# Performance work log

Hardware: AMD Instinct MI355X
Metric: run time of the kernel (lower is better)

The kernel has to match this reference:

```python
import jax, jax.numpy as jnp
import numpy as np

M_RANGE = 3
K = 2 * M_RANGE + 1          # kernel size = 7
N_CLASS = K * K              # 49 motion classes
IM_CHANNEL = 3


def setup_inputs() -> dict:
    key = jax.random.key(0)
    k1, k2, k3, k4 = jax.random.split(key, 4)
    B, H, W = 16, 256, 256
    im_input = jax.random.normal(k1, (B, 2 * IM_CHANNEL, H, W), dtype=jnp.float32)
    im_output = jax.random.normal(k2, (B, IM_CHANNEL, H, W), dtype=jnp.float32)
    # motion in [-M_RANGE, M_RANGE-1) so that floor(m)+M_RANGE+1 <= K-1 (valid bin)
    gt_motion = jax.random.uniform(k3, (B, 2, H, W), dtype=jnp.float32) * (2 * M_RANGE - 1) - M_RANGE
    # grouped-conv weight (already in post-swapaxes [n_class, 1, K, K] layout)
    m_kernel = jax.random.uniform(k4, (N_CLASS, 1, K, K), dtype=jnp.float32)
    return {"im_input": im_input, "im_output": im_output,
            "gt_motion": gt_motion, "m_kernel": m_kernel}


def _axis_weights(m):
    # m: [B,H,W] -> bilinear binning weights over K bins: [B,H,W,K]
    f = jnp.floor(m)
    frac = m - f
    idx = f.astype(jnp.int32) + M_RANGE
    oh0 = jax.nn.one_hot(idx, K, dtype=m.dtype)
    oh1 = jax.nn.one_hot(idx + 1, K, dtype=m.dtype)
    return (1.0 - frac)[..., None] * oh0 + frac[..., None] * oh1


def motion2mask(motion):
    # faithful vectorization of the triple-loop: mask[c=iy*K+ix] = b[iy]*a[ix]
    ax = _axis_weights(motion[:, 0])   # x-motion -> columns of ger(b, a)
    ay = _axis_weights(motion[:, 1])   # y-motion -> rows
    mask = ay[..., :, None] * ax[..., None, :]       # [B,H,W,K,K] outer product
    B, H, W = motion.shape[0], motion.shape[2], motion.shape[3]
    return mask.reshape(B, H, W, N_CLASS).transpose(0, 3, 1, 2)  # [B,N_CLASS,H,W]


def _conv(x, w, groups):
    return jax.lax.conv_general_dilated(
        x, w, window_strides=(1, 1),
        padding=[(M_RANGE, M_RANGE), (M_RANGE, M_RANGE)],
        dimension_numbers=("NCHW", "OIHW", "NCHW"),
        feature_group_count=groups)


def reference(im_input, im_output, gt_motion, m_kernel):
    m_mask = motion2mask(gt_motion)                   # [B,N_CLASS,H,W]
    out_mask = _conv(m_mask, m_kernel, N_CLASS)       # grouped conv, same shape
    im = im_input[:, -IM_CHANNEL:]                    # [B,3,H,W]
    B, C, H, W = im.shape
    # construct_image: each channel expanded to N_CLASS copies then grouped-conv
    # == plain conv of each single channel with all N_CLASS kernels
    nearby = _conv(im.reshape(B * C, 1, H, W), m_kernel, 1)
    nearby = nearby.reshape(B, C, N_CLASS, H, W)
    pred = (nearby * out_mask[:, None]).sum(axis=2)   # [B,3,H,W]
    return pred, m_mask
```

## Files before the change

kernel.cpp:

```cpp
#include <hip/hip_runtime.h>
#include <hip/hip_fp16.h>

typedef _Float16 f16x8 __attribute__((ext_vector_type(8)));
typedef float    f32x4 __attribute__((ext_vector_type(4)));

#define TILE   16
#define HALO   22
#define KK     7
#define NCLASS 49
#define IMW    256
#define IMH    256
#define HW     65536
#define HH     484
#define NV     42
#define WST    52

#define OFF_OMV    0
#define OFF_HALOW  10752
#define OFF_HALON  11720
#define OFF_KV     12204
#define OFF_KE     14262
#define OFF_IML64  15488
#define OFF_IML32  16456
#define SH_TOTAL   16940

__device__ __forceinline__ unsigned h2u(__half2 h) { union { __half2 h; unsigned u; } c; c.h = h; return c.u; }
__device__ __forceinline__ __half2  u2h(unsigned u) { union { __half2 h; unsigned u; } c; c.u = u; return c.h; }

__global__ __launch_bounds__(256, 2)
void gtnet_kernel(const float* __restrict__ im_input,
                  const float* __restrict__ gt_motion,
                  const float* __restrict__ m_kernel,
                  float* __restrict__ out_pred,
                  float* __restrict__ out_mask)
{
    __shared__ __align__(16) unsigned SH[SH_TOTAL];
    unsigned* const omV   = SH + OFF_OMV;
    uint2*   const haloW  = (uint2*)(SH + OFF_HALOW);
    unsigned* const haloN = SH + OFF_HALON;
    unsigned* const KV    = SH + OFF_KV;
    unsigned* const KE    = SH + OFF_KE;
    float2*  const iml64  = (float2*)(SH + OFF_IML64);
    float*   const iml32  = (float*)(SH + OFF_IML32);
    float*   const Wf     = (float*)SH;

    const int tid  = threadIdx.x;
    const int lane = tid & 63, wv_id = tid >> 6;
    const int tx = tid & 15, ty = tid >> 4;
    const int x0 = blockIdx.x * TILE, y0 = blockIdx.y * TILE;
    const int b  = blockIdx.z;
    const int x = x0 + tx, y = y0 + ty;

    for (int i = tid; i < NCLASS * NV; i += 256) {
        int s = i / NV, n = i - s * NV;
        float k0 = m_kernel[n * NCLASS + s];
        float k7 = m_kernel[(n + KK) * NCLASS + s];
        KV[i] = h2u(__halves2half2(__float2half_rn(k0), __float2half_rn(k7)));
    }
    for (int i = tid; i < NCLASS * 25; i += 256) {
        int t = i / 25, j = i - t * 25;
        float k0 = m_kernel[(2 * j) * NCLASS + t];
        float k1 = (2 * j + 1 < NCLASS) ? m_kernel[(2 * j + 1) * NCLASS + t] : 0.0f;
        KE[i] = h2u(__halves2half2(__float2half_rn(k0), __float2half_rn(k1)));
    }

    const float* mot_x = gt_motion + (size_t)b * 2 * HW;
    const float* mot_y = mot_x + HW;
    for (int i = tid; i < HH; i += 256) {
        int hy = i / HALO, hx = i - hy * HALO;
        int gy = y0 - 3 + hy, gx = x0 - 3 + hx;
        uint2 wv2 = make_uint2(0u, 0u);
        unsigned n4 = 0;
        if (gy >= 0 && gy < IMH && gx >= 0 && gx < IMW) {
            int off = gy * IMW + gx;
            float ay = mot_y[off] + 3.0f;
            float ax = mot_x[off] + 3.0f;
            float iyf = floorf(ay), ixf = floorf(ax);
            float fy = ay - iyf,    fx = ax - ixf;
            int n00 = (int)iyf * KK + (int)ixf;
            n00 = (n00 < 0) ? 0 : ((n00 > 40) ? 40 : n00);
            wv2.x = h2u(__halves2half2(__float2half_rn(1.0f - fy), __float2half_rn(fy)));
            wv2.y = h2u(__halves2half2(__float2half_rn(1.0f - fx), __float2half_rn(fx)));
            n4 = (unsigned)(n00 * 4);
        }
        haloW[i] = wv2;
        haloN[i] = n4;
    }

    const float* imP = im_input + ((size_t)b * 6 + 3) * HW;
    for (int i = tid; i < HH; i += 256) {
        int hy = i / HALO, hx = i - hy * HALO;
        int gy = y0 - 3 + hy, gx = x0 - 3 + hx;
        float2 v01 = make_float2(0.0f, 0.0f);
        float  v2  = 0.0f;
        if (gy >= 0 && gy < IMH && gx >= 0 && gx < IMW) {
            int off = gy * IMW + gx;
            v01.x = imP[off];
            v01.y = imP[off + HW];
            v2    = imP[off + 2 * HW];
        }
        iml64[i] = v01;
        iml32[i] = v2;
    }

    {
        uint4* p = reinterpret_cast<uint4*>(omV);
        for (int i = tid; i < (2 * NV * 128) / 4; i += 256) p[i] = make_uint4(0, 0, 0, 0);
    }

    __syncthreads();

    {
        int off = y * IMW + x;
        float ay = mot_y[off] + 3.0f;
        float ax = mot_x[off] + 3.0f;
        float iyf = floorf(ay), ixf = floorf(ax);
        float fy = ay - iyf,    fx = ax - ixf;
        int   iy = (int)iyf,    ix = (int)ixf;
        float wyA[KK], wxB[KK];
        #pragma unroll
        for (int a = 0; a < KK; a++) {
            wyA[a] = (a == iy) ? (1.0f - fy) : ((a == iy + 1) ? fy : 0.0f);
            wxB[a] = (a == ix) ? (1.0f - fx) : ((a == ix + 1) ? fx : 0.0f);
        }
        float* mm = out_mask + (size_t)b * NCLASS * HW + off;
        #pragma unroll
        for (int a = 0; a < KK; a++)
            #pragma unroll
            for (int bb = 0; bb < KK; bb++)
                mm[(size_t)(a * KK + bb) * HW] = wyA[a] * wxB[bb];
    }

    unsigned* const omHalf = omV + (tid >> 7) * (NV * 128) + (tid & 127);
    #pragma unroll
    for (int u = 0; u < KK; u++) {
        #pragma unroll
        for (int v = 0; v < KK; v++) {
            const int s = u * KK + v;
            const int q = (ty + u) * HALO + (tx + v);
            uint2 wyx = haloW[q];
            unsigned n4 = haloN[q];
            const unsigned* kp =
                (const unsigned*)((const char*)KV + s * (NV * 4) + n4);
            unsigned kvA = kp[0], kvB = kp[1];
            unsigned* ob = (unsigned*)((char*)omHalf + n4 * 128);
            unsigned o0 = ob[0], o1 = ob[128];
            __half2 wy = u2h(wyx.x), wx = u2h(wyx.y);
            __half2 cA = __hmul2(__hmul2(wy, __low2half2(wx)),  u2h(kvA));
            __half2 cB = __hmul2(__hmul2(wy, __high2half2(wx)), u2h(kvB));
            ob[0]   = h2u(__hadd2(u2h(o0), cA));
            ob[128] = h2u(__hadd2(u2h(o1), cB));
        }
    }

    __syncthreads();

    f16x8 af[2][4];
    #pragma unroll
    for (int kit = 0; kit < 2; kit++) {
        #pragma unroll
        for (int mt = 0; mt < 4; mt++) {
            int k0  = kit * 32 + (lane >> 4) * 8;
            int px  = wv_id * 64 + mt * 16 + (lane & 15);
            const unsigned* pxb = omV + (px >> 7) * (NV * 128) + (px & 127);
            union { unsigned u[4]; f16x8 v; } au;
            #pragma unroll
            for (int j = 0; j < 4; j++) {
                int c0 = k0 + 2 * j;
                int rl = (c0 > 40) ? 40 : c0;
                unsigned d0 = pxb[rl * 128], d1 = pxb[rl * 128 + 128];
                unsigned loM = (d0 & 0xffffu) | (d1 << 16);
                loM = (c0 <= 40) ? loM : 0u;
                int r0 = c0 - 7; r0 = (r0 < 0) ? 0 : ((r0 > 41) ? 41 : r0);
                int r1 = c0 - 6; r1 = (r1 < 0) ? 0 : ((r1 > 41) ? 41 : r1);
                unsigned e0 = pxb[r0 * 128];
                unsigned e1 = pxb[r1 * 128];
                e0 = (c0 >= 8 && c0 <= 48) ? e0 : 0u;
                e1 = (c0 >= 6 && c0 <= 48) ? e1 : 0u;
                unsigned hiM = (e0 >> 16) | (e1 & 0xffff0000u);
                au.u[j] = h2u(__hadd2(u2h(loM), u2h(hiM)));
            }
            af[kit][mt] = au.v;
        }
    }
    f16x8 bfr[2][4];
    #pragma unroll
    for (int kit = 0; kit < 2; kit++) {
        #pragma unroll
        for (int nt = 0; nt < 4; nt++) {
            int t  = nt * 16 + (lane & 15);
            int k0 = kit * 32 + (lane >> 4) * 8;
            union { unsigned u[4]; f16x8 v; } bu;
            #pragma unroll
            for (int j = 0; j < 4; j++) {
                int c0 = k0 + 2 * j;
                int j2 = c0 >> 1;
                unsigned val = KE[t * 25 + ((j2 > 24) ? 24 : j2)];
                bu.u[j] = (c0 <= 48) ? val : 0u;
            }
            bfr[kit][nt] = bu.v;
        }
    }

    __syncthreads();

    f32x4 acc[4][4];
    #pragma unroll
    for (int mt = 0; mt < 4; mt++) {
        #pragma unroll
        for (int nt = 0; nt < 4; nt++) {
            f32x4 c = {0.0f, 0.0f, 0.0f, 0.0f};
            c = __builtin_amdgcn_mfma_f32_16x16x32_f16(af[0][mt], bfr[0][nt], c, 0, 0, 0);
            c = __builtin_amdgcn_mfma_f32_16x16x32_f16(af[1][mt], bfr[1][nt], c, 0, 0, 0);
            acc[mt][nt] = c;
        }
    }

    #pragma unroll
    for (int mt = 0; mt < 4; mt++) {
        #pragma unroll
        for (int nt = 0; nt < 4; nt++) {
            int t = nt * 16 + (lane & 15);
            if (t < NCLASS) {
                #pragma unroll
                for (int r = 0; r < 4; r++) {
                    int px = wv_id * 64 + mt * 16 + (lane >> 4) * 4 + r;
                    Wf[px * WST + t] = acc[mt][nt][r];
                }
            }
        }
    }

    __syncthreads();

    float wv[NCLASS];
    #pragma unroll
    for (int t = 0; t < NCLASS; t++) wv[t] = Wf[tid * WST + t];

    float a0 = 0.0f, a1 = 0.0f, a2 = 0.0f;
    #pragma unroll
    for (int p = 0; p < KK; p++) {
        #pragma unroll
        for (int q = 0; q < KK; q++) {
            float wvv = wv[p * KK + q];
            int   hi = (ty + p) * HALO + (tx + q);
            float2 i01 = iml64[hi];
            float  i2  = iml32[hi];
            a0 = fmaf(wvv, i01.x, a0);
            a1 = fmaf(wvv, i01.y, a1);
            a2 = fmaf(wvv, i2,    a2);
        }
    }
    float* pr = out_pred + (size_t)b * 3 * HW + y * IMW + x;
    pr[0]      = a0;
    pr[HW]     = a1;
    pr[2 * HW] = a2;
}

extern "C" void kernel_launch(void* const* d_in, const int* in_sizes, int n_in,
                              void* d_out, int out_size, void* d_ws, size_t ws_size,
                              hipStream_t stream) {
    const float* im_input  = (const float*)d_in[0];
    const float* gt_motion = (const float*)d_in[2];
    const float* m_kernel  = (const float*)d_in[3];

    float* pred = (float*)d_out;
    float* mask = pred + (size_t)16 * 3 * HW;

    dim3 grid(IMW / TILE, IMH / TILE, 16);
    dim3 block(256);
    hipLaunchKernelGGL(gtnet_kernel, grid, block, 0, stream,
                       im_input, gt_motion, m_kernel, pred, mask);
}
```

Baseline: 337.9 us.

## Shrink shared memory footprint to raise occupancy to three blocks per CU

```diff
diff --git a/kernel.cpp b/kernel.cpp
--- a/kernel.cpp
+++ b/kernel.cpp
@@ -13,21 +13,20 @@
 #define HW     65536
 #define HH     484
 #define NV     42
-#define WST    52
+#define WHST   52
 
 #define OFF_OMV    0
-#define OFF_HALOW  10752
-#define OFF_HALON  11720
-#define OFF_KV     12204
-#define OFF_KE     14262
-#define OFF_IML64  15488
-#define OFF_IML32  16456
-#define SH_TOTAL   16940
+#define OFF_HALOF  10752
+#define OFF_HALOB  11236
+#define OFF_KV     11357
+#define SH_TOTAL   13415
+#define OFF_IML64  10752
+#define OFF_IML32  11720
 
 __device__ __forceinline__ unsigned h2u(__half2 h) { union { __half2 h; unsigned u; } c; c.h = h; return c.u; }
 __device__ __forceinline__ __half2  u2h(unsigned u) { union { __half2 h; unsigned u; } c; c.u = u; return c.h; }
 
-__global__ __launch_bounds__(256, 2)
+__global__ __launch_bounds__(256, 3)
 void gtnet_kernel(const float* __restrict__ im_input,
                   const float* __restrict__ gt_motion,
                   const float* __restrict__ m_kernel,
@@ -35,14 +34,13 @@
                   float* __restrict__ out_mask)
 {
     __shared__ __align__(16) unsigned SH[SH_TOTAL];
-    unsigned* const omV   = SH + OFF_OMV;
-    uint2*   const haloW  = (uint2*)(SH + OFF_HALOW);
-    unsigned* const haloN = SH + OFF_HALON;
-    unsigned* const KV    = SH + OFF_KV;
-    unsigned* const KE    = SH + OFF_KE;
-    float2*  const iml64  = (float2*)(SH + OFF_IML64);
-    float*   const iml32  = (float*)(SH + OFF_IML32);
-    float*   const Wf     = (float*)SH;
+    unsigned*      const omV    = SH + OFF_OMV;
+    unsigned*      const haloF  = SH + OFF_HALOF;
+    unsigned char* const haloB8 = (unsigned char*)(SH + OFF_HALOB);
+    unsigned*      const KV     = SH + OFF_KV;
+    float2*        const iml64  = (float2*)(SH + OFF_IML64);
+    float*         const iml32  = (float*)(SH + OFF_IML32);
+    __half*        const Whf    = (__half*)SH;
 
     const int tid  = threadIdx.x;
     const int lane = tid & 63, wv_id = tid >> 6;
@@ -51,58 +49,56 @@
     const int b  = blockIdx.z;
     const int x = x0 + tx, y = y0 + ty;
 
+    const float* mot_x = gt_motion + (size_t)b * 2 * HW;
+    const float* mot_y = mot_x + HW;
+    const float* imP   = im_input + ((size_t)b * 6 + 3) * HW;
+
+    float2 imr01[2]; float imr2[2];
+    #pragma unroll
+    for (int k = 0; k < 2; k++) {
+        int i = tid + k * 256;
+        float2 v01 = make_float2(0.0f, 0.0f); float v2 = 0.0f;
+        if (i < HH) {
+            int hy = i / HALO, hx = i - hy * HALO;
+            int gy = y0 - 3 + hy, gx = x0 - 3 + hx;
+            if (gy >= 0 && gy < IMH && gx >= 0 && gx < IMW) {
+                int off = gy * IMW + gx;
+                v01.x = imP[off];
+                v01.y = imP[off + HW];
+                v2    = imP[off + 2 * HW];
+            }
+        }
+        imr01[k] = v01; imr2[k] = v2;
+    }
+
     for (int i = tid; i < NCLASS * NV; i += 256) {
         int s = i / NV, n = i - s * NV;
         float k0 = m_kernel[n * NCLASS + s];
         float k7 = m_kernel[(n + KK) * NCLASS + s];
         KV[i] = h2u(__halves2half2(__float2half_rn(k0), __float2half_rn(k7)));
     }
-    for (int i = tid; i < NCLASS * 25; i += 256) {
-        int t = i / 25, j = i - t * 25;
-        float k0 = m_kernel[(2 * j) * NCLASS + t];
-        float k1 = (2 * j + 1 < NCLASS) ? m_kernel[(2 * j + 1) * NCLASS + t] : 0.0f;
-        KE[i] = h2u(__halves2half2(__float2half_rn(k0), __float2half_rn(k1)));
-    }
-
-    const float* mot_x = gt_motion + (size_t)b * 2 * HW;
-    const float* mot_y = mot_x + HW;
-    for (int i = tid; i < HH; i += 256) {
-        int hy = i / HALO, hx = i - hy * HALO;
-        int gy = y0 - 3 + hy, gx = x0 - 3 + hx;
-        uint2 wv2 = make_uint2(0u, 0u);
-        unsigned n4 = 0;
-        if (gy >= 0 && gy < IMH && gx >= 0 && gx < IMW) {
-            int off = gy * IMW + gx;
-            float ay = mot_y[off] + 3.0f;
-            float ax = mot_x[off] + 3.0f;
-            float iyf = floorf(ay), ixf = floorf(ax);
-            float fy = ay - iyf,    fx = ax - ixf;
-            int n00 = (int)iyf * KK + (int)ixf;
-            n00 = (n00 < 0) ? 0 : ((n00 > 40) ? 40 : n00);
-            wv2.x = h2u(__halves2half2(__float2half_rn(1.0f - fy), __float2half_rn(fy)));
-            wv2.y = h2u(__halves2half2(__float2half_rn(1.0f - fx), __float2half_rn(fx)));
-            n4 = (unsigned)(n00 * 4);
-        }
-        haloW[i] = wv2;
-        haloN[i] = n4;
-    }
-
-    const float* imP = im_input + ((size_t)b * 6 + 3) * HW;
-    for (int i = tid; i < HH; i += 256) {
-        int hy = i / HALO, hx = i - hy * HALO;
-        int gy = y0 - 3 + hy, gx = x0 - 3 + hx;
-        float2 v01 = make_float2(0.0f, 0.0f);
-        float  v2  = 0.0f;
-        if (gy >= 0 && gy < IMH && gx >= 0 && gx < IMW) {
-            int off = gy * IMW + gx;
-            v01.x = imP[off];
-            v01.y = imP[off + HW];
-            v2    = imP[off + 2 * HW];
-        }
-        iml64[i] = v01;
-        iml32[i] = v2;
-    }
-
+    #pragma unroll
+    for (int k = 0; k < 2; k++) {
+        int i = tid + k * 256;
+        if (i < HH) {
+            int hy = i / HALO, hx = i - hy * HALO;
+            int gy = y0 - 3 + hy, gx = x0 - 3 + hx;
+            unsigned pf = 0u, n4b = 255u;
+            if (gy >= 0 && gy < IMH && gx >= 0 && gx < IMW) {
+                int off = gy * IMW + gx;
+                float ay = mot_y[off] + 3.0f;
+                float ax = mot_x[off] + 3.0f;
+                float iyf = floorf(ay), ixf = floorf(ax);
+                float fy = ay - iyf,    fx = ax - ixf;
+                int n00 = (int)iyf * KK + (int)ixf;
+                n00 = (n00 < 0) ? 0 : ((n00 > 40) ? 40 : n00);
+                pf  = h2u(__halves2half2(__float2half_rn(fy), __float2half_rn(fx)));
+                n4b = (unsigned)(n00 * 4);
+            }
+            haloF[i]  = pf;
+            haloB8[i] = (unsigned char)n4b;
+        }
+    }
     {
         uint4* p = reinterpret_cast<uint4*>(omV);
         for (int i = tid; i < (2 * NV * 128) / 4; i += 256) p[i] = make_uint4(0, 0, 0, 0);
@@ -132,28 +128,62 @@
     }
 
     unsigned* const omHalf = omV + (tid >> 7) * (NV * 128) + (tid & 127);
+    const __half hone = __float2half_rn(1.0f);
     #pragma unroll
     for (int u = 0; u < KK; u++) {
         #pragma unroll
         for (int v = 0; v < KK; v++) {
             const int s = u * KK + v;
             const int q = (ty + u) * HALO + (tx + v);
-            uint2 wyx = haloW[q];
-            unsigned n4 = haloN[q];
+            unsigned pf  = haloF[q];
+            unsigned n4u = (unsigned)haloB8[q];
+            unsigned n4  = (n4u == 255u) ? 0u : n4u;
+            __half2 f2 = u2h(pf);
+            __half fy = __low2half(f2), fx = __high2half(f2);
+            unsigned wyb = h2u(__halves2half2(__hsub(hone, fy), fy));
+            wyb = (n4u == 255u) ? 0u : wyb;
+            __half2 wy  = u2h(wyb);
+            __half2 wxl = __half2half2(__hsub(hone, fx));
+            __half2 wxh = __half2half2(fx);
             const unsigned* kp =
                 (const unsigned*)((const char*)KV + s * (NV * 4) + n4);
             unsigned kvA = kp[0], kvB = kp[1];
             unsigned* ob = (unsigned*)((char*)omHalf + n4 * 128);
             unsigned o0 = ob[0], o1 = ob[128];
-            __half2 wy = u2h(wyx.x), wx = u2h(wyx.y);
-            __half2 cA = __hmul2(__hmul2(wy, __low2half2(wx)),  u2h(kvA));
-            __half2 cB = __hmul2(__hmul2(wy, __high2half2(wx)), u2h(kvB));
+            __half2 cA = __hmul2(__hmul2(wy, wxl), u2h(kvA));
+            __half2 cB = __hmul2(__hmul2(wy, wxh), u2h(kvB));
             ob[0]   = h2u(__hadd2(u2h(o0), cA));
             ob[128] = h2u(__hadd2(u2h(o1), cB));
         }
     }
 
     __syncthreads();
+
+    #pragma unroll
+    for (int k = 0; k < 2; k++) {
+        int i = tid + k * 256;
+        if (i < HH) { iml64[i] = imr01[k]; iml32[i] = imr2[k]; }
+    }
+
+    f16x8 bfr[2][4];
+    #pragma unroll
+    for (int kit = 0; kit < 2; kit++) {
+        #pragma unroll
+        for (int nt = 0; nt < 4; nt++) {
+            int t  = nt * 16 + (lane & 15);
+            int tc = (t > 48) ? 48 : t;
+            int k0 = kit * 32 + (lane >> 4) * 8;
+            union { unsigned u[4]; f16x8 v; } bu;
+            #pragma unroll
+            for (int j = 0; j < 4; j++) {
+                int c0 = k0 + 2 * j;
+                float lo = (c0 <= 48) ? m_kernel[c0 * NCLASS + tc]       : 0.0f;
+                float hi = (c0 <= 47) ? m_kernel[(c0 + 1) * NCLASS + tc] : 0.0f;
+                bu.u[j] = h2u(__halves2half2(__float2half_rn(lo), __float2half_rn(hi)));
+            }
+            bfr[kit][nt] = bu.v;
+        }
+    }
 
     f16x8 af[2][4];
     #pragma unroll
@@ -183,24 +213,6 @@
             af[kit][mt] = au.v;
         }
     }
-    f16x8 bfr[2][4];
-    #pragma unroll
-    for (int kit = 0; kit < 2; kit++) {
-        #pragma unroll
-        for (int nt = 0; nt < 4; nt++) {
-            int t  = nt * 16 + (lane & 15);
-            int k0 = kit * 32 + (lane >> 4) * 8;
-            union { unsigned u[4]; f16x8 v; } bu;
-            #pragma unroll
-            for (int j = 0; j < 4; j++) {
-                int c0 = k0 + 2 * j;
-                int j2 = c0 >> 1;
-                unsigned val = KE[t * 25 + ((j2 > 24) ? 24 : j2)];
-                bu.u[j] = (c0 <= 48) ? val : 0u;
-            }
-            bfr[kit][nt] = bu.v;
-        }
-    }
 
     __syncthreads();
 
@@ -225,7 +237,7 @@
                 #pragma unroll
                 for (int r = 0; r < 4; r++) {
                     int px = wv_id * 64 + mt * 16 + (lane >> 4) * 4 + r;
-                    Wf[px * WST + t] = acc[mt][nt][r];
+                    Whf[px * WHST + t] = __float2half_rn(acc[mt][nt][r]);
                 }
             }
         }
@@ -233,19 +245,20 @@
 
     __syncthreads();
 
-    float wv[NCLASS];
-    #pragma unroll
-    for (int t = 0; t < NCLASS; t++) wv[t] = Wf[tid * WST + t];
+    union { uint2 v[13]; __half h[52]; } wr;
+    const uint2* wp = (const uint2*)(Whf + tid * WHST);
+    #pragma unroll
+    for (int c = 0; c < 13; c++) wr.v[c] = wp[c];
 
     float a0 = 0.0f, a1 = 0.0f, a2 = 0.0f;
     #pragma unroll
     for (int p = 0; p < KK; p++) {
         #pragma unroll
-        for (int q = 0; q < KK; q++) {
-            float wvv = wv[p * KK + q];
-            int   hi = (ty + p) * HALO + (tx + q);
-            float2 i01 = iml64[hi];
-            float  i2  = iml32[hi];
+        for (int qq = 0; qq < KK; qq++) {
+            float wvv = __half2float(wr.h[p * KK + qq]);
+            int   hq  = (ty + p) * HALO + (tx + qq);
+            float2 i01 = iml64[hq];
+            float  i2  = iml32[hq];
             a0 = fmaf(wvv, i01.x, a0);
             a1 = fmaf(wvv, i01.y, a1);
             a2 = fmaf(wvv, i2,    a2);
```

New measurement: 343.7 us. No clear change (+1.7%).
